# Kernel tuning notes

Measured on AMD Instinct MI355X. Metric: run time of the kernel, lower is better.

The kernel has to match this reference:

```python
import jax, jax.numpy as jnp
import numpy as np

ALPHA = 0.5  # torch forward default alpha


def setup_inputs() -> dict:
    key = jax.random.key(0)
    k1, k2, k3 = jax.random.split(key, 3)
    N, D, C = 16384, 2048, 1000
    group_x = jax.random.normal(k1, (N, D), dtype=jnp.float32)
    mu = jax.random.normal(k2, (C, D), dtype=jnp.float32)
    group_y = jax.random.randint(k3, (N,), 0, C, dtype=jnp.int64)
    return {"group_x": group_x, "group_y": group_y, "mu": mu}


def reference(group_x, group_y, mu):
    # Mahalanobis-style distance from original m_distance:
    # sqrt( diag((x - mu_c)(x - mu_c)^T) / 2 ) == sqrt(||x - mu_c||^2 / 2)
    # Computed directly (O(N*D*C) GEMM) instead of the original's O(N^2*D*C)
    # full pairwise matmul + diagonal extraction -- identical math.
    C = mu.shape[0]
    x_sq = jnp.sum(group_x * group_x, axis=1, keepdims=True)        # [N,1]
    mu_sq = jnp.sum(mu * mu, axis=1)[None, :]                        # [1,C]
    cross = jnp.einsum('nd,cd->nc', group_x, mu)                     # [N,C]
    sq_dist = jnp.maximum(x_sq - 2.0 * cross + mu_sq, 0.0)           # [N,C]
    distance = jnp.sqrt(sq_dist * 0.5)                               # [N,C]

    label_onehot = jax.nn.one_hot(group_y, C, dtype=distance.dtype)  # [N,C]
    adjust = distance * (1.0 + ALPHA * label_onehot)                 # [N,C]

    # F.cross_entropy(-adjust, group_y): mean NLL of log_softmax(-adjust)
    logp = jax.nn.log_softmax(-adjust, axis=1)                       # [N,C]
    picked = jnp.take_along_axis(logp, group_y[:, None], axis=1)[:, 0]
    return -jnp.mean(picked)
```

## Files before the change

### kernel.cpp

```cpp
#include <hip/hip_runtime.h>

typedef float f32x4  __attribute__((ext_vector_type(4)));
typedef int   i32x4  __attribute__((ext_vector_type(4)));
typedef int   i32x8  __attribute__((ext_vector_type(8)));

__device__ inline void gload_lds16(const void* g, void* l) {
    __builtin_amdgcn_global_load_lds((const __attribute__((address_space(1))) void*)g,
                                     (__attribute__((address_space(3))) void*)l,
                                     16, 0, 0);
}

__device__ inline unsigned int enc_fp4(float v) {
    float a = fabsf(v);
    unsigned int c = (unsigned int)(a > 0.25f) + (a > 0.75f) + (a > 1.25f) +
                     (a > 1.75f) + (a > 2.5f)  + (a > 3.5f)  + (a > 5.0f);
    return c | ((v < 0.f) ? 8u : 0u);
}

__global__ __launch_bounds__(256) void convert_kernel(
        const float* __restrict__ x, const float* __restrict__ mu,
        unsigned int* __restrict__ x4, unsigned int* __restrict__ mu4,
        float* __restrict__ x_sq, float* __restrict__ mu_sq,
        int D, int N, int C, int Cpad) {
    const int bid = blockIdx.x;
    const int t = threadIdx.x;
    const bool isX = bid < N;
    const int r = isX ? bid : bid - N;

    unsigned int* out = (isX ? x4 : mu4) + (size_t)r * (D / 8) + t;
    if (!isX && r >= C) {
        *out = 0u;
        if (t == 0) mu_sq[r] = 0.f;
        return;
    }
    const float* src = (isX ? x + (size_t)r * D : mu + (size_t)r * D) + t * 8;
    float4 v0 = *(const float4*)(src);
    float4 v1 = *(const float4*)(src + 4);
    float acc = v0.x * v0.x + v0.y * v0.y + v0.z * v0.z + v0.w * v0.w
              + v1.x * v1.x + v1.y * v1.y + v1.z * v1.z + v1.w * v1.w;
    unsigned int p = enc_fp4(v0.x) | (enc_fp4(v0.y) << 4) | (enc_fp4(v0.z) << 8)
                   | (enc_fp4(v0.w) << 12) | (enc_fp4(v1.x) << 16)
                   | (enc_fp4(v1.y) << 20) | (enc_fp4(v1.z) << 24)
                   | (enc_fp4(v1.w) << 28);
    *out = p;

    for (int off = 32; off; off >>= 1) acc += __shfl_down(acc, off, 64);
    __shared__ float sbuf[4];
    if ((t & 63) == 0) sbuf[t >> 6] = acc;
    __syncthreads();
    if (t == 0) {
        float s = sbuf[0] + sbuf[1] + sbuf[2] + sbuf[3];
        if (isX) x_sq[r] = s; else mu_sq[r] = s;
    }
}

#define BM 256
#define BN 256
#define BKE 256

__global__ __launch_bounds__(512, 2) void gemm_fused_kernel(
        const unsigned char* __restrict__ A,
        const unsigned char* __restrict__ B,
        const float* __restrict__ x_sq, const float* __restrict__ mu_sq,
        const int* __restrict__ y,
        float* __restrict__ pM, float* __restrict__ pS, float* __restrict__ pP,
        int Kb, int C, int NCB) {
    __shared__ __align__(16) char smem[131072];

    const int t  = threadIdx.x;
    const int l  = t & 63, w = t >> 6;
    const int wr = w >> 2, wc = w & 3;
    const int lr = l & 15, kh = l >> 4;
    const int rowBase = blockIdx.x * BM;
    const int colBase = blockIdx.y * BN;
    const int nt = (Kb * 2) / BKE;

    const int lc = (t & 7) ^ ((t >> 3) & 7);
    const unsigned char* gA = A + (size_t)(rowBase + (t >> 3)) * Kb + lc * 16;
    const unsigned char* gB = B + (size_t)(colBase + (t >> 3)) * Kb + lc * 16;

    auto STAGE = [&](int q) {
        const int qc = (q < nt) ? q : nt - 1;
        char* dst = smem + (q & 1) * 65536 + t * 16;
        const unsigned char* ga = gA + (size_t)qc * 128;
        const unsigned char* gb = gB + (size_t)qc * 128;
#pragma unroll
        for (int r = 0; r < 4; ++r)
            gload_lds16(ga + (size_t)r * 64 * Kb, dst + r * 8192);
#pragma unroll
        for (int r = 0; r < 4; ++r)
            gload_lds16(gb + (size_t)r * 64 * Kb, dst + 32768 + r * 8192);
    };

    const int aRow = (wr * 128 + lr) * 128;
    const int bRow = 32768 + (wc * 64 + lr) * 128;
    const int swz = (lr & 7);

    f32x4 acc[8][4];
#pragma unroll
    for (int m = 0; m < 8; ++m)
#pragma unroll
        for (int n = 0; n < 4; ++n) acc[m][n] = (f32x4){0.f, 0.f, 0.f, 0.f};

    STAGE(0);
    asm volatile("s_waitcnt vmcnt(0)" ::: "memory");
    __builtin_amdgcn_s_barrier();

    const int SC = 0x7f7f7f7f;

#pragma unroll 1
    for (int q = 0; q < nt; ++q) {
        STAGE(q + 1);
        const char* buf = smem + (q & 1) * 65536;
#pragma unroll
        for (int s = 0; s < 2; ++s) {
            const int ch = ((s * 4 + kh) ^ swz) << 4;
            i32x4 aF[8], bF[4];
#pragma unroll
            for (int m = 0; m < 8; ++m)
                aF[m] = *(const i32x4*)(buf + aRow + m * 2048 + ch);
#pragma unroll
            for (int n = 0; n < 4; ++n)
                bF[n] = *(const i32x4*)(buf + bRow + n * 2048 + ch);
            asm volatile("s_waitcnt lgkmcnt(0)" ::: "memory");
            __builtin_amdgcn_sched_barrier(0);
            __builtin_amdgcn_s_setprio(1);
#pragma unroll
            for (int m = 0; m < 8; ++m) {
                i32x8 a8 = __builtin_shufflevector(aF[m], aF[m], 0, 1, 2, 3, 0, 1, 2, 3);
#pragma unroll
                for (int n = 0; n < 4; ++n) {
                    i32x8 b8 = __builtin_shufflevector(bF[n], bF[n], 0, 1, 2, 3, 0, 1, 2, 3);
                    acc[m][n] = __builtin_amdgcn_mfma_scale_f32_16x16x128_f8f6f4(
                        a8, b8, acc[m][n], 4 , 4 , 0, SC, 0, SC);
                }
            }
            __builtin_amdgcn_s_setprio(0);
        }
        asm volatile("s_waitcnt vmcnt(0)" ::: "memory");
        __builtin_amdgcn_s_barrier();
    }

    __syncthreads();
    float (*part)[4][3] = (float(*)[4][3])smem;

#pragma unroll
    for (int m = 0; m < 8; ++m) {
#pragma unroll
        for (int j = 0; j < 4; ++j) {
            const int row_l = wr * 128 + m * 16 + kh * 4 + j;
            const int grow = rowBase + row_l;
            const float xs = x_sq[grow];
            const int yr = y[grow];
            float v[4];
            float vmax = -3.4e38f, pick = -1.f;
#pragma unroll
            for (int n = 0; n < 4; ++n) {
                const int col = colBase + wc * 64 + n * 16 + lr;
                const float cr = acc[m][n][j];
                const float sq = fmaxf(xs - 2.f * cr + mu_sq[col], 0.f) * 0.5f;
                const float dd = sqrtf(sq);
                const float adj = (col == yr) ? 1.5f * dd : dd;
                if (col == yr) pick = adj;
                v[n] = (col < C) ? -adj : -1e30f;
                vmax = fmaxf(vmax, v[n]);
            }
            for (int off = 1; off <= 8; off <<= 1)
                vmax = fmaxf(vmax, __shfl_xor(vmax, off, 64));
            float s = 0.f;
#pragma unroll
            for (int n = 0; n < 4; ++n) s += expf(v[n] - vmax);
            for (int off = 1; off <= 8; off <<= 1) s += __shfl_xor(s, off, 64);
            for (int off = 1; off <= 8; off <<= 1)
                pick = fmaxf(pick, __shfl_xor(pick, off, 64));
            if (lr == 0) {
                part[row_l][wc][0] = vmax;
                part[row_l][wc][1] = s;
                part[row_l][wc][2] = pick;
            }
        }
    }
    __syncthreads();
    if (t < 256) {
        float Mx = part[t][0][0], S = 0.f, pk = part[t][0][2];
#pragma unroll
        for (int b = 1; b < 4; ++b) Mx = fmaxf(Mx, part[t][b][0]);
#pragma unroll
        for (int b = 0; b < 4; ++b) {
            S += part[t][b][1] * expf(part[t][b][0] - Mx);
            pk = fmaxf(pk, part[t][b][2]);
        }
        const size_t o = (size_t)(rowBase + t) * NCB + blockIdx.y;
        pM[o] = Mx; pS[o] = S; pP[o] = pk;
    }
}

__global__ __launch_bounds__(256) void loss_combine_kernel(
        const float* __restrict__ pM, const float* __restrict__ pS,
        const float* __restrict__ pP, float* __restrict__ bsum, int NCB) {
    const int t = threadIdx.x;
    const int row = blockIdx.x * 256 + t;
    float Mx = -3.4e38f;
    for (int b = 0; b < NCB; ++b) Mx = fmaxf(Mx, pM[(size_t)row * NCB + b]);
    float S = 0.f, pick = -1.f;
    for (int b = 0; b < NCB; ++b) {
        S += pS[(size_t)row * NCB + b] * expf(pM[(size_t)row * NCB + b] - Mx);
        pick = fmaxf(pick, pP[(size_t)row * NCB + b]);
    }
    float loss = pick + logf(S) + Mx;
    for (int off = 32; off; off >>= 1) loss += __shfl_down(loss, off, 64);
    __shared__ float sb[4];
    if ((t & 63) == 0) sb[t >> 6] = loss;
    __syncthreads();
    if (t == 0) bsum[blockIdx.x] = sb[0] + sb[1] + sb[2] + sb[3];
}

__global__ __launch_bounds__(64) void final_mean_kernel(
        const float* __restrict__ bsum, float* __restrict__ out, int nb, int N) {
    float a = 0.f;
    for (int i = threadIdx.x; i < nb; i += 64) a += bsum[i];
    for (int off = 32; off; off >>= 1) a += __shfl_down(a, off, 64);
    if (threadIdx.x == 0) out[0] = a / (float)N;
}

extern "C" void kernel_launch(void* const* d_in, const int* in_sizes, int n_in,
                              void* d_out, int out_size, void* d_ws, size_t ws_size,
                              hipStream_t stream) {
    const float* x  = (const float*)d_in[0];
    const int*   y  = (const int*)d_in[1];
    const float* mu = (const float*)d_in[2];

    const int N = in_sizes[1];
    const int D = in_sizes[0] / N;
    const int C = in_sizes[2] / D;
    const int Cpad = ((C + 255) / 256) * 256;
    const int NCB = Cpad / BN;
    const int NRB = N / 256;
    const int Kb = D / 2;

    char* ws = (char*)d_ws;
    unsigned char* x4  = (unsigned char*)ws;  ws += (size_t)N * Kb;
    unsigned char* mu4 = (unsigned char*)ws;  ws += (size_t)Cpad * Kb;
    float* x_sq  = (float*)ws;                ws += (size_t)N * 4;
    float* mu_sq = (float*)ws;                ws += (size_t)Cpad * 4;
    float* pM    = (float*)ws;                ws += (size_t)N * NCB * 4;
    float* pS    = (float*)ws;                ws += (size_t)N * NCB * 4;
    float* pP    = (float*)ws;                ws += (size_t)N * NCB * 4;
    float* bsum  = (float*)ws;                ws += (size_t)NRB * 4;

    convert_kernel<<<N + Cpad, 256, 0, stream>>>(
        x, mu, (unsigned int*)x4, (unsigned int*)mu4, x_sq, mu_sq, D, N, C, Cpad);
    gemm_fused_kernel<<<dim3(N / BM, Cpad / BN), 512, 0, stream>>>(
        x4, mu4, x_sq, mu_sq, y, pM, pS, pP, Kb, C, NCB);
    loss_combine_kernel<<<NRB, 256, 0, stream>>>(pM, pS, pP, bsum, NCB);
    final_mean_kernel<<<1, 64, 0, stream>>>(bsum, d_out ? (float*)d_out : nullptr, NRB, N);
}
```

Measured before the change: 75.04 us.

## Switch GEMM mainloop to triple-buffered LDS with smaller K-tiles

Result: slower. 76.55 us (+2.0%).

```diff
diff --git a/kernel.cpp b/kernel.cpp
--- a/kernel.cpp
+++ b/kernel.cpp
@@ -56,7 +56,6 @@
 
 #define BM 256
 #define BN 256
-#define BKE 256
 
 __global__ __launch_bounds__(512, 2) void gemm_fused_kernel(
         const unsigned char* __restrict__ A,
@@ -65,7 +64,7 @@
         const int* __restrict__ y,
         float* __restrict__ pM, float* __restrict__ pS, float* __restrict__ pP,
         int Kb, int C, int NCB) {
-    __shared__ __align__(16) char smem[131072];
+    __shared__ __align__(16) char smem[98304];
 
     const int t  = threadIdx.x;
     const int l  = t & 63, w = t >> 6;
@@ -73,28 +72,27 @@
     const int lr = l & 15, kh = l >> 4;
     const int rowBase = blockIdx.x * BM;
     const int colBase = blockIdx.y * BN;
-    const int nt = (Kb * 2) / BKE;
-
-    const int lc = (t & 7) ^ ((t >> 3) & 7);
-    const unsigned char* gA = A + (size_t)(rowBase + (t >> 3)) * Kb + lc * 16;
-    const unsigned char* gB = B + (size_t)(colBase + (t >> 3)) * Kb + lc * 16;
+    const int nt = Kb / 64;
+
+    const int lc = (t & 3) ^ ((t >> 2) & 3);
+    const unsigned char* gA = A + (size_t)(rowBase + (t >> 2)) * Kb + lc * 16;
+    const unsigned char* gB = B + (size_t)(colBase + (t >> 2)) * Kb + lc * 16;
 
     auto STAGE = [&](int q) {
         const int qc = (q < nt) ? q : nt - 1;
-        char* dst = smem + (q & 1) * 65536 + t * 16;
-        const unsigned char* ga = gA + (size_t)qc * 128;
-        const unsigned char* gb = gB + (size_t)qc * 128;
-#pragma unroll
-        for (int r = 0; r < 4; ++r)
-            gload_lds16(ga + (size_t)r * 64 * Kb, dst + r * 8192);
-#pragma unroll
-        for (int r = 0; r < 4; ++r)
-            gload_lds16(gb + (size_t)r * 64 * Kb, dst + 32768 + r * 8192);
+        char* dst = smem + (q % 3) * 32768 + t * 16;
+        const size_t ko = (size_t)qc * 64;
+#pragma unroll
+        for (int r = 0; r < 2; ++r)
+            gload_lds16(gA + ko + (size_t)r * 128 * Kb, dst + r * 8192);
+#pragma unroll
+        for (int r = 0; r < 2; ++r)
+            gload_lds16(gB + ko + (size_t)r * 128 * Kb, dst + 16384 + r * 8192);
     };
 
-    const int aRow = (wr * 128 + lr) * 128;
-    const int bRow = 32768 + (wc * 64 + lr) * 128;
-    const int swz = (lr & 7);
+    const int pch = (kh ^ (lr & 3)) << 4;
+    const int aBase = (wr * 128 + lr) * 64 + pch;
+    const int bBase = 16384 + (wc * 64 + lr) * 64 + pch;
 
     f32x4 acc[8][4];
 #pragma unroll
@@ -102,45 +100,42 @@
 #pragma unroll
         for (int n = 0; n < 4; ++n) acc[m][n] = (f32x4){0.f, 0.f, 0.f, 0.f};
 
-    STAGE(0);
-    asm volatile("s_waitcnt vmcnt(0)" ::: "memory");
+    const int SC = 0x7f7f7f7f;
+
+    STAGE(0); STAGE(1);
+    asm volatile("s_waitcnt vmcnt(4)" ::: "memory");
     __builtin_amdgcn_s_barrier();
-
-    const int SC = 0x7f7f7f7f;
 
 #pragma unroll 1
     for (int q = 0; q < nt; ++q) {
-        STAGE(q + 1);
-        const char* buf = smem + (q & 1) * 65536;
-#pragma unroll
-        for (int s = 0; s < 2; ++s) {
-            const int ch = ((s * 4 + kh) ^ swz) << 4;
-            i32x4 aF[8], bF[4];
-#pragma unroll
-            for (int m = 0; m < 8; ++m)
-                aF[m] = *(const i32x4*)(buf + aRow + m * 2048 + ch);
-#pragma unroll
-            for (int n = 0; n < 4; ++n)
-                bF[n] = *(const i32x4*)(buf + bRow + n * 2048 + ch);
-            asm volatile("s_waitcnt lgkmcnt(0)" ::: "memory");
-            __builtin_amdgcn_sched_barrier(0);
-            __builtin_amdgcn_s_setprio(1);
-#pragma unroll
-            for (int m = 0; m < 8; ++m) {
-                i32x8 a8 = __builtin_shufflevector(aF[m], aF[m], 0, 1, 2, 3, 0, 1, 2, 3);
-#pragma unroll
-                for (int n = 0; n < 4; ++n) {
-                    i32x8 b8 = __builtin_shufflevector(bF[n], bF[n], 0, 1, 2, 3, 0, 1, 2, 3);
-                    acc[m][n] = __builtin_amdgcn_mfma_scale_f32_16x16x128_f8f6f4(
-                        a8, b8, acc[m][n], 4 , 4 , 0, SC, 0, SC);
-                }
+        STAGE(q + 2);
+        const char* buf = smem + (q % 3) * 32768;
+        i32x4 aF[8], bF[4];
+#pragma unroll
+        for (int m = 0; m < 8; ++m)
+            aF[m] = *(const i32x4*)(buf + aBase + m * 1024);
+#pragma unroll
+        for (int n = 0; n < 4; ++n)
+            bF[n] = *(const i32x4*)(buf + bBase + n * 1024);
+        asm volatile("s_waitcnt lgkmcnt(0)" ::: "memory");
+        __builtin_amdgcn_sched_barrier(0);
+        __builtin_amdgcn_s_setprio(1);
+#pragma unroll
+        for (int m = 0; m < 8; ++m) {
+            i32x8 a8 = __builtin_shufflevector(aF[m], aF[m], 0, 1, 2, 3, 0, 1, 2, 3);
+#pragma unroll
+            for (int n = 0; n < 4; ++n) {
+                i32x8 b8 = __builtin_shufflevector(bF[n], bF[n], 0, 1, 2, 3, 0, 1, 2, 3);
+                acc[m][n] = __builtin_amdgcn_mfma_scale_f32_16x16x128_f8f6f4(
+                    a8, b8, acc[m][n], 4 , 4 , 0, SC, 0, SC);
             }
-            __builtin_amdgcn_s_setprio(0);
         }
-        asm volatile("s_waitcnt vmcnt(0)" ::: "memory");
+        __builtin_amdgcn_s_setprio(0);
+        asm volatile("s_waitcnt vmcnt(4)" ::: "memory");
         __builtin_amdgcn_s_barrier();
     }
 
+    asm volatile("s_waitcnt vmcnt(0)" ::: "memory");
     __syncthreads();
     float (*part)[4][3] = (float(*)[4][3])smem;
 
```
